# Optimization experiments

Hardware: AMD Instinct MI355X
Metric: run time of the kernel (lower is better)

Reference implementation:

```python
import jax, jax.numpy as jnp
import numpy as np
import math

MAX_L = 2
TARGET_DIM = 64


def build_transform_matrix(target_dim=TARGET_DIM, max_l=MAX_L):
    """Replicates WignerTransformMatrix._build_transform_matrix: [target_dim^2, 9]."""
    wigner_dims = [2 * l + 1 for l in range(max_l + 1)]  # [1, 3, 5]
    T = np.zeros((target_dim * target_dim, 9), dtype=np.float32)
    start = 0
    for l in range(max_l + 1):
        d = wigner_dims[l]
        if l == 0:
            for i in range(3):
                T[start, i * 3 + i] = 1.0 / 3.0
        elif l == 1:
            for i in range(d):
                for j in range(d):
                    T[start + i * d + j, i * 3 + j] = 1.0
        elif l == 2:
            for i in range(min(d, 3)):
                T[start + i * d + i, i * 3 + i] = 1.0
            rules = [(0, 1, [(0, 1, 0.5), (1, 0, 0.5)]),
                     (0, 2, [(0, 2, 0.7), (2, 0, 0.3)]),
                     (1, 2, [(1, 2, 0.6), (2, 1, 0.4)]),
                     (0, 4, [(0, 1, 0.3), (1, 0, 0.3), (0, 2, 0.2), (2, 0, 0.2)])]
            for oi, oj, combos in rules:
                if oi < d and oj < d:
                    for ii, jj, w in combos:
                        T[start + oi * d + oj, ii * 3 + jj] = w
                        if oi != oj:
                            T[start + oj * d + oi, ii * 3 + jj] = w
        start += d * d
    return jnp.asarray(T)


def setup_inputs() -> dict:
    key = jax.random.key(0)
    ks = jax.random.split(key, 12)
    B, N, H, G, D = 2, 1024, 8, 2, 64
    s = 0.02
    return {
        "x": jax.random.normal(ks[0], (B, N, H, G, D), dtype=jnp.float32),
        "rotations": jax.random.normal(ks[1], (B, N, 3, 3), dtype=jnp.float32),
        "mask": jnp.ones((B, N), dtype=bool),
        "Wq": jax.random.normal(ks[2], (D, D), dtype=jnp.float32) * s,
        "bq": jnp.zeros((D,), dtype=jnp.float32),
        "Wk": jax.random.normal(ks[3], (D, D), dtype=jnp.float32) * s,
        "bk": jnp.zeros((D,), dtype=jnp.float32),
        "Wv": jax.random.normal(ks[4], (D, D), dtype=jnp.float32) * s,
        "bv": jnp.zeros((D,), dtype=jnp.float32),
        "Wo": jax.random.normal(ks[5], (D, D), dtype=jnp.float32) * s,
        "bo": jnp.zeros((D,), dtype=jnp.float32),
        "fusion_weight": jnp.ones((1,), dtype=jnp.float32),
    }


def reference(x, rotations, mask, Wq, bq, Wk, bk, Wv, bv, Wo, bo, fusion_weight):
    B, N, H, G, D = x.shape
    HG = H * G
    scale = math.sqrt(D)
    T = build_transform_matrix(D, MAX_L)  # [D*D, 9]

    # projections (torch Linear: x @ W.T + b)
    q = (x @ Wq.T + bq).reshape(B, N, HG, D).transpose(0, 2, 1, 3)  # [B,HG,N,D]
    k = (x @ Wk.T + bk).reshape(B, N, HG, D).transpose(0, 2, 1, 3)
    v = (x @ Wv.T + bv).reshape(B, N, HG, D).transpose(0, 2, 1, 3)

    scores = jnp.einsum('bhnd,bhmd->bhnm', q, k) / scale  # [B,HG,N,N]

    # Wigner matrices: vec(R) @ T.T -> [B,N,D,D]
    R_vec = rotations.reshape(B, N, 9)
    wig = (R_vec @ T.T).reshape(B, N, D, D)

    # per-token transformed q/k (no [B,HG,N,D,D] materialization)
    q_t = jnp.einsum('bhnd,bnde->bhne', q, wig)
    k_t = jnp.einsum('bhnd,bnde->bhne', k, wig)
    wigner_scores = jnp.einsum('bhnd,bhmd->bhnm', q_t, k_t) / scale

    enhanced = scores + fusion_weight[0] * wigner_scores
    mask2d = mask[:, None, :, None] & mask[:, None, None, :]  # [B,1,N,N]
    enhanced = jnp.where(mask2d, enhanced, -jnp.inf)

    attn = jax.nn.softmax(enhanced, axis=-1)
    out = jnp.einsum('bhnm,bhmd->bhnd', attn, v)  # [B,HG,N,D]
    out = out.transpose(0, 2, 1, 3).reshape(B, N, H, G, D)
    return out @ Wo.T + bo
```

## Files before the change

### kernel.cpp

```cpp
#include <hip/hip_runtime.h>
#include <cstring>
#include <cstddef>

#define NB  2
#define NN  1024
#define NHG 16
#define ND  64

typedef unsigned short ushort_t;
typedef __attribute__((ext_vector_type(8))) short short8v;
typedef __attribute__((ext_vector_type(16))) float f32x16;

struct MMat { float m[81]; };

#define L2E 1.44269504088896f

__device__ inline unsigned cvt_pk_bf16(float a, float b) {
  unsigned r;
  asm("v_cvt_pk_bf16_f32 %0, %1, %2" : "=v"(r) : "v"(a), "v"(b));
  return r;
}
__device__ inline void split_pair(float a, float b, unsigned& hw, unsigned& lw) {
  hw = cvt_pk_bf16(a, b);
  float ah = __uint_as_float(hw << 16);
  float bh = __uint_as_float(hw & 0xffff0000u);
  lw = cvt_pk_bf16(a - ah, b - bh);
}

__device__ inline f32x16 mfma32(short8v a, short8v b, f32x16 c) {
  return __builtin_amdgcn_mfma_f32_32x32x16_bf16(a, b, c, 0, 0, 0);
}

__device__ inline void gl_lds16(const ushort_t* g, ushort_t* l) {
  __builtin_amdgcn_global_load_lds(
      (const __attribute__((address_space(1))) void*)g,
      (__attribute__((address_space(3))) void*)l, 16, 0, 0);
}

static void compute_M(float* M) {
  static float T[4096][9];
  std::memset(T, 0, sizeof(T));
  int start = 0;
  for (int l = 0; l <= 2; ++l) {
    int d = 2 * l + 1;
    if (l == 0) {
      for (int i = 0; i < 3; ++i) T[start][i * 3 + i] = 1.0f / 3.0f;
    } else if (l == 1) {
      for (int i = 0; i < d; ++i)
        for (int j = 0; j < d; ++j)
          T[start + i * d + j][i * 3 + j] = 1.0f;
    } else {
      for (int i = 0; i < 3; ++i) T[start + i * d + i][i * 3 + i] = 1.0f;
      const int   oiA[4] = {0, 0, 1, 0}, ojA[4] = {1, 2, 2, 4};
      const int   cnt_[4] = {2, 2, 2, 4};
      const int   iiA[4][4] = {{0,1,0,0},{0,2,0,0},{1,2,0,0},{0,1,0,2}};
      const int   jjA[4][4] = {{1,0,0,0},{2,0,0,0},{2,1,0,0},{1,0,2,0}};
      const float wA[4][4]  = {{0.5f,0.5f,0,0},{0.7f,0.3f,0,0},{0.6f,0.4f,0,0},{0.3f,0.3f,0.2f,0.2f}};
      for (int r = 0; r < 4; ++r) {
        int oi = oiA[r], oj = ojA[r];
        if (oi < d && oj < d) {
          for (int c = 0; c < cnt_[r]; ++c) {
            T[start + oi * d + oj][iiA[r][c] * 3 + jjA[r][c]] = wA[r][c];
            if (oi != oj) T[start + oj * d + oi][iiA[r][c] * 3 + jjA[r][c]] = wA[r][c];
          }
        }
      }
    }
    start += d * d;
  }
  for (int i = 0; i < 9; ++i)
    for (int j = 0; j < 9; ++j) {
      double a = 0.0;
      for (int f = 0; f < 4096; ++f) a += (double)T[f][i] * (double)T[f][j];
      M[i * 9 + j] = (float)a;
    }
}

__global__ __launch_bounds__(256) void qkv_gemm(
    const float* __restrict__ x, const float* __restrict__ rot,
    const float* __restrict__ fusion,
    const float* __restrict__ Wq, const float* __restrict__ bq,
    const float* __restrict__ Wk, const float* __restrict__ bk,
    const float* __restrict__ Wv, const float* __restrict__ bv,
    ushort_t* __restrict__ Qb, ushort_t* __restrict__ Kb,
    ushort_t* __restrict__ VhT, MMat Mm) {
  const int tid = threadIdx.x;
  const int w = tid >> 6, l = tid & 63;
  const int l31 = l & 31, hi5 = l >> 5;
  const int mt = blockIdx.x, p = blockIdx.y;
  const int bh = mt >> 3, n0 = (mt & 7) << 7;
  const float* W    = p == 0 ? Wq : (p == 1 ? Wk : Wv);
  const float* bvec = p == 0 ? bq : (p == 1 ? bk : bv);

  __shared__ union UU {
    struct { ushort_t A[128 * 72]; ushort_t B[2][64 * 72]; } s;
    float D[128 * 67];
  } u;
  __shared__ float biasS[64];
  __shared__ float rotS[128][9];

  #pragma unroll
  for (int it = 0; it < 8; ++it) {
    int i = tid + it * 256;
    int r = i >> 4, c4 = i & 15;
    const float* src = x + (((size_t)((bh >> 4) * 1024 + n0 + r) * 16 + (bh & 15)) << 6) + (c4 << 2);
    float4 v = *(const float4*)src;
    uint2 hw = { cvt_pk_bf16(v.x, v.y), cvt_pk_bf16(v.z, v.w) };
    *(uint2*)(&u.s.A[r * 72 + c4 * 4]) = hw;
  }
  #pragma unroll
  for (int it = 0; it < 4; ++it) {
    int i = tid + it * 256;
    int r = i >> 4, c4 = i & 15;
    float4 v = *(const float4*)(W + ((size_t)i << 2));
    unsigned h0, l0, h1, l1;
    split_pair(v.x, v.y, h0, l0);
    split_pair(v.z, v.w, h1, l1);
    uint2 hw = { h0, h1 }, lw = { l0, l1 };
    *(uint2*)(&u.s.B[0][r * 72 + c4 * 4]) = hw;
    *(uint2*)(&u.s.B[1][r * 72 + c4 * 4]) = lw;
  }
  if (tid < 64) biasS[tid] = bvec[tid];
  if (p < 2) {
    for (int i = tid; i < 1152; i += 256) {
      int r = i / 9, c = i - r * 9;
      rotS[r][c] = rot[((size_t)((bh >> 4) * 1024 + n0 + r)) * 9 + c];
    }
  }
  __syncthreads();

  f32x16 acc0, acc1;
  #pragma unroll
  for (int r = 0; r < 16; ++r) { acc0[r] = 0.f; acc1[r] = 0.f; }
  const int mbase = w << 5;
  __builtin_amdgcn_s_setprio(1);
  #pragma unroll
  for (int s = 0; s < 4; ++s) {
    const int ko = s * 16 + 8 * hi5;
    short8v aH  = *(const short8v*)(&u.s.A[(mbase + l31) * 72 + ko]);
    short8v b0H = *(const short8v*)(&u.s.B[0][l31 * 72 + ko]);
    short8v b0L = *(const short8v*)(&u.s.B[1][l31 * 72 + ko]);
    short8v b1H = *(const short8v*)(&u.s.B[0][(32 + l31) * 72 + ko]);
    short8v b1L = *(const short8v*)(&u.s.B[1][(32 + l31) * 72 + ko]);
    acc0 = mfma32(aH, b0H, acc0);
    acc0 = mfma32(aH, b0L, acc0);
    acc1 = mfma32(aH, b1H, acc1);
    acc1 = mfma32(aH, b1L, acc1);
  }
  __builtin_amdgcn_s_setprio(0);
  __syncthreads();
  #pragma unroll
  for (int r = 0; r < 16; ++r) {
    int m = mbase + (r & 3) + 8 * (r >> 2) + 4 * hi5;
    u.D[m * 67 + l31]      = acc0[r];
    u.D[m * 67 + 32 + l31] = acc1[r];
  }
  __syncthreads();

  if (p < 2) {
    const int mloc = tid >> 1, dh = (tid & 1) << 5;
    ushort_t* dst = p ? Kb : Qb;
    const float scale = p ? 1.0f : 0.125f * L2E;
    const size_t rowo = ((size_t)bh * 1024 + n0 + mloc) * 80;
    #pragma unroll
    for (int j = 0; j < 4; ++j) {
      union { unsigned wd[4]; short8v v; } pk;
      #pragma unroll
      for (int e = 0; e < 4; ++e) {
        int c = dh + 8 * j + 2 * e;
        float v0 = (u.D[mloc * 67 + c]     + biasS[c])     * scale;
        float v1 = (u.D[mloc * 67 + c + 1] + biasS[c + 1]) * scale;
        pk.wd[e] = cvt_pk_bf16(v0, v1);
      }
      *(short8v*)(dst + rowo + dh + 8 * j) = pk.v;
    }
    if (dh == 0) {
      float base0 = u.D[mloc * 67] + biasS[0];
      float e16[16];
      if (p == 0) {
        float fq = fusion[0] * base0 * (0.125f * L2E);
        #pragma unroll
        for (int j = 0; j < 16; ++j) e16[j] = (j < 9) ? fq * rotS[mloc][j] : 0.f;
      } else {
        #pragma unroll
        for (int j = 0; j < 16; ++j) {
          float a = 0.f;
          if (j < 9) {
            #pragma unroll
            for (int jj = 0; jj < 9; ++jj)
              a = fmaf(Mm.m[j * 9 + jj], rotS[mloc][jj], a);
          }
          e16[j] = base0 * a;
        }
      }
      union { unsigned wd[4]; short8v v; } pa, pb;
      #pragma unroll
      for (int e = 0; e < 4; ++e) {
        pa.wd[e] = cvt_pk_bf16(e16[2 * e], e16[2 * e + 1]);
        pb.wd[e] = cvt_pk_bf16(e16[8 + 2 * e], e16[9 + 2 * e]);
      }
      *(short8v*)(dst + rowo + 64) = pa.v;
      *(short8v*)(dst + rowo + 72) = pb.v;
    }
  } else {
    const int d = tid >> 2, nb = tid & 3;
    const float bd = biasS[d];
    const size_t ob = ((size_t)bh * 64 + d) * 1024 + n0;
    #pragma unroll
    for (int j = 0; j < 4; ++j) {
      int chunk = nb * 4 + j;
      union { unsigned wd[4]; short8v v; } pk;
      #pragma unroll
      for (int e = 0; e < 4; ++e) {
        int c = chunk * 8 + 2 * e;
        float v0 = u.D[c * 67 + d] + bd;
        float v1 = u.D[(c + 1) * 67 + d] + bd;
        pk.wd[e] = cvt_pk_bf16(v0, v1);
      }
      int slot = (chunk & 8) | ((chunk & 7) ^ (d & 7));
      *(short8v*)(VhT + ob + slot * 8) = pk.v;
    }
  }
}

__global__ __launch_bounds__(256, 4) void attn_kernel(
    const ushort_t* __restrict__ Qb, const ushort_t* __restrict__ Kb,
    const ushort_t* __restrict__ VhT,
    unsigned* __restrict__ OpartW, float* __restrict__ Ml, int SPLIT, int KTN) {
  const int tid = threadIdx.x;
  const int w = tid >> 6, l = tid & 63;
  const int l31 = l & 31, hi5 = l >> 5;
  const int bid = blockIdx.x;
  const int bh = bid & 31, rest = bid >> 5;
  const int qt = rest & 7, sp = rest >> 3;
  const int qn0 = qt * 128 + w * 32;
  const int sl = l31 & 7;

  __shared__ ushort_t Ks[2][64 * 80];
  __shared__ ushort_t Vs[2][64 * 64];

  short8v qh[5];
  {
    const ushort_t* qrow = Qb + ((size_t)bh * 1024 + qn0 + l31) * 80;
    #pragma unroll
    for (int s = 0; s < 5; ++s)
      qh[s] = *(const short8v*)(qrow + 16 * s + 8 * hi5);
  }

  f32x16 Ob0, Ob1;
  #pragma unroll
  for (int r = 0; r < 16; ++r) { Ob0[r] = 0.f; Ob1[r] = 0.f; }
  float lsum = 0.f;

  const ushort_t* Kbase = Kb + (size_t)bh * 1024 * 80;
  const ushort_t* VhB = VhT + (size_t)bh * 65536;
  const int kv0 = sp * KTN * 64;

  auto stage = [&](int b, int kt) {
    const int kb = kv0 + kt * 64;
    #pragma unroll
    for (int j = 0; j < 3; ++j) {
      int i = tid + j * 256;
      if (i < 640)
        gl_lds16(Kbase + (size_t)(kb + i / 10) * 80 + (i % 10) * 8, &Ks[b][i * 8]);
    }
    #pragma unroll
    for (int j = 0; j < 2; ++j) {
      int i = tid + j * 256;
      gl_lds16(VhB + (size_t)(i >> 3) * 1024 + kb + (i & 7) * 8, &Vs[b][i * 8]);
    }
  };

  stage(0, 0);
  for (int kt = 0; kt < KTN; ++kt) {
    const int cur = kt & 1;
    const bool haveNext = (kt + 1 < KTN);
    if (haveNext) stage(cur ^ 1, kt + 1);
    if (!haveNext)  { asm volatile("s_waitcnt vmcnt(0)" ::: "memory"); }
    else if (w < 2) { asm volatile("s_waitcnt vmcnt(5)" ::: "memory"); }
    else            { asm volatile("s_waitcnt vmcnt(4)" ::: "memory"); }
    __builtin_amdgcn_sched_barrier(0);
    __builtin_amdgcn_s_barrier();

    f32x16 S0, S1;
    #pragma unroll
    for (int r = 0; r < 16; ++r) { S0[r] = 0.f; S1[r] = 0.f; }
    __builtin_amdgcn_s_setprio(1);
    #pragma unroll
    for (int s = 0; s < 5; ++s) {
      short8v ka0 = *(const short8v*)(&Ks[cur][l31 * 80 + (2 * s + hi5) * 8]);
      S0 = mfma32(ka0, qh[s], S0);
      short8v ka1 = *(const short8v*)(&Ks[cur][(32 + l31) * 80 + (2 * s + hi5) * 8]);
      S1 = mfma32(ka1, qh[s], S1);
    }
    __builtin_amdgcn_s_setprio(0);

    float p0[16], p1[16];
    float ps = 0.f;
    #pragma unroll
    for (int r = 0; r < 16; ++r) {
      p0[r] = __builtin_amdgcn_exp2f(S0[r]);
      p1[r] = __builtin_amdgcn_exp2f(S1[r]);
      ps += p0[r] + p1[r];
    }
    lsum += ps;

    #pragma unroll
    for (int B = 0; B < 2; ++B) {
      const float* pp = (B == 0) ? p0 : p1;
      unsigned wh[8];
      #pragma unroll
      for (int i = 0; i < 8; ++i) wh[i] = cvt_pk_bf16(pp[2 * i], pp[2 * i + 1]);
      __builtin_amdgcn_s_setprio(1);
      #pragma unroll
      for (int s = 0; s < 2; ++s) {
        unsigned a0 = wh[4 * s], a1 = wh[4 * s + 1];
        unsigned b0 = wh[4 * s + 2], b1 = wh[4 * s + 3];
        asm volatile("v_permlane32_swap_b32 %0, %1" : "+v"(a0), "+v"(b0));
        asm volatile("v_permlane32_swap_b32 %0, %1" : "+v"(a1), "+v"(b1));
        union U8 { short8v v; unsigned u[4]; } aph;
        aph.u[0] = a0; aph.u[1] = a1; aph.u[2] = b0; aph.u[3] = b1;
        int slot = 4 * B + 2 * s + hi5;
        short8v vH0 = *(const short8v*)(&Vs[cur][l31 * 64 + (slot ^ sl) * 8]);
        Ob0 = mfma32(aph.v, vH0, Ob0);
        short8v vH1 = *(const short8v*)(&Vs[cur][(32 + l31) * 64 + (slot ^ sl) * 8]);
        Ob1 = mfma32(aph.v, vH1, Ob1);
      }
      __builtin_amdgcn_s_setprio(0);
    }
    __builtin_amdgcn_s_barrier();
  }

  lsum += __shfl_xor(lsum, 32, 64);
  #pragma unroll
  for (int r = 0; r < 16; ++r) {
    int cr = (r & 3) + 8 * (r >> 2) + 4 * hi5;
    size_t rowb = ((size_t)(bh * 1024 + qn0 + cr) * SPLIT + sp) * 32;
    OpartW[rowb + l31] = cvt_pk_bf16(Ob0[r], Ob1[r]);
  }
  if (l < 32)
    Ml[(size_t)(bh * 1024 + qn0 + l) * SPLIT + sp] = lsum;
}

__global__ __launch_bounds__(256) void oproj_gemm(
    const unsigned* __restrict__ OpartW, const float* __restrict__ Ml,
    float* __restrict__ out,
    const float* __restrict__ Wo, const float* __restrict__ bo, int SPLIT) {
  const int tid = threadIdx.x;
  const int w = tid >> 6, l = tid & 63;
  const int l31 = l & 31, hi5 = l >> 5;
  const int m0 = blockIdx.x << 6;
  const int rh = (w & 1) << 5;
  const int ch = (w >> 1) << 5;

  __shared__ union UU {
    struct { ushort_t A[64 * 72]; ushort_t B[2][64 * 72]; } s;
    float D[64 * 67];
  } u;
  __shared__ float biasS[64];
  __shared__ float cf[64];

  if (tid < 64) {
    int row = m0 + tid;
    int n = (row >> 4) & 1023, hgb = row & 15, bb = row >> 14;
    size_t prow = ((size_t)(bb * 16 + hgb)) * 1024 + n;
    float lt = 0.f;
    for (int s = 0; s < SPLIT; ++s) lt += Ml[prow * SPLIT + s];
    cf[tid] = 1.0f / lt;
  }
  if (tid >= 192) biasS[tid - 192] = bo[tid - 192];
  __syncthreads();

  #pragma unroll
  for (int it = 0; it < 2; ++it) {
    int i = tid + it * 256;
    int r = i >> 3, q4 = i & 7;
    int row = m0 + r;
    int n = (row >> 4) & 1023, hgb = row & 15, bb = row >> 14;
    size_t prow = ((size_t)(bb * 16 + hgb)) * 1024 + n;
    float f[8] = {0.f, 0.f, 0.f, 0.f, 0.f, 0.f, 0.f, 0.f};
    for (int s = 0; s < SPLIT; ++s) {
      uint4 wv = *(const uint4*)(OpartW + (prow * SPLIT + s) * 32 + q4 * 4);
      unsigned wa[4] = { wv.x, wv.y, wv.z, wv.w };
      #pragma unroll
      for (int j = 0; j < 4; ++j) {
        f[j]     += __uint_as_float(wa[j] << 16);
        f[4 + j] += __uint_as_float(wa[j] & 0xffff0000u);
      }
    }
    float li = cf[r];
    #pragma unroll
    for (int j = 0; j < 8; ++j) f[j] *= li;
    uint2 lo = { cvt_pk_bf16(f[0], f[1]), cvt_pk_bf16(f[2], f[3]) };
    uint2 hi = { cvt_pk_bf16(f[4], f[5]), cvt_pk_bf16(f[6], f[7]) };
    *(uint2*)(&u.s.A[r * 72 + q4 * 4])      = lo;
    *(uint2*)(&u.s.A[r * 72 + 32 + q4 * 4]) = hi;
  }
  #pragma unroll
  for (int it = 0; it < 4; ++it) {
    int i = tid + it * 256;
    int r = i >> 4, c4 = i & 15;
    float4 v = *(const float4*)(Wo + ((size_t)i << 2));
    unsigned h0, l0, h1, l1;
    split_pair(v.x, v.y, h0, l0);
    split_pair(v.z, v.w, h1, l1);
    uint2 hw = { h0, h1 }, lw = { l0, l1 };
    *(uint2*)(&u.s.B[0][r * 72 + c4 * 4]) = hw;
    *(uint2*)(&u.s.B[1][r * 72 + c4 * 4]) = lw;
  }
  __syncthreads();

  f32x16 acc;
  #pragma unroll
  for (int r = 0; r < 16; ++r) acc[r] = 0.f;
  __builtin_amdgcn_s_setprio(1);
  #pragma unroll
  for (int s = 0; s < 4; ++s) {
    const int ko = s * 16 + 8 * hi5;
    short8v aH = *(const short8v*)(&u.s.A[(rh + l31) * 72 + ko]);
    short8v bH = *(const short8v*)(&u.s.B[0][(ch + l31) * 72 + ko]);
    short8v bL = *(const short8v*)(&u.s.B[1][(ch + l31) * 72 + ko]);
    acc = mfma32(aH, bH, acc);
    acc = mfma32(aH, bL, acc);
  }
  __builtin_amdgcn_s_setprio(0);
  __syncthreads();
  #pragma unroll
  for (int r = 0; r < 16; ++r) {
    int m = rh + (r & 3) + 8 * (r >> 2) + 4 * hi5;
    u.D[m * 67 + ch + l31] = acc[r];
  }
  __syncthreads();

  const int mloc = tid >> 2, q = tid & 3;
  float* orow = out + ((size_t)(m0 + mloc) << 6) + q * 16;
  #pragma unroll
  for (int j = 0; j < 4; ++j) {
    int c = q * 16 + 4 * j;
    float4 v;
    v.x = u.D[mloc * 67 + c + 0] + biasS[c + 0];
    v.y = u.D[mloc * 67 + c + 1] + biasS[c + 1];
    v.z = u.D[mloc * 67 + c + 2] + biasS[c + 2];
    v.w = u.D[mloc * 67 + c + 3] + biasS[c + 3];
    *(float4*)(orow + 4 * j) = v;
  }
}

extern "C" void kernel_launch(void* const* d_in, const int* in_sizes, int n_in,
                              void* d_out, int out_size, void* d_ws, size_t ws_size,
                              hipStream_t stream) {
  const float* x   = (const float*)d_in[0];
  const float* rot = (const float*)d_in[1];
  const float* Wq  = (const float*)d_in[3];
  const float* bq  = (const float*)d_in[4];
  const float* Wk  = (const float*)d_in[5];
  const float* bk  = (const float*)d_in[6];
  const float* Wv  = (const float*)d_in[7];
  const float* bv  = (const float*)d_in[8];
  const float* Wo  = (const float*)d_in[9];
  const float* bo  = (const float*)d_in[10];
  const float* fus = (const float*)d_in[11];
  float* out = (float*)d_out;
  char* ws = (char*)d_ws;

  ushort_t* Qb  = (ushort_t*)ws;
  ushort_t* Kb  = (ushort_t*)(ws + 5242880);
  ushort_t* VhT = (ushort_t*)(ws + 10485760);
  const size_t obase = 14680064;

  int SPLIT = 1;
  if (ws_size >= obase + 4 * 4325376) SPLIT = 4;
  else if (ws_size >= obase + 2 * 4325376) SPLIT = 2;
  const int KTN = 16 / SPLIT;
  unsigned* OpartW = (unsigned*)(ws + obase);
  float*    Ml     = (float*)(ws + obase + (size_t)4194304 * SPLIT);

  MMat Mm;
  compute_M(Mm.m);

  qkv_gemm<<<dim3(256, 3), 256, 0, stream>>>(x, rot, fus, Wq, bq, Wk, bk, Wv, bv,
                                             Qb, Kb, VhT, Mm);
  attn_kernel<<<256 * SPLIT, 256, 0, stream>>>(Qb, Kb, VhT, OpartW, Ml, SPLIT, KTN);
  oproj_gemm<<<512, 256, 0, stream>>>(OpartW, Ml, out, Wo, bo, SPLIT);
}
```

Baseline: 46.52 us.

## Process two query tiles per attention block to reuse staged K/V tiles

Each attention block now handles two 128-row query tiles (A and B) against the same staged K/V tiles in LDS. This halves the block count and the global-to-LDS K/V traffic per query row, at the cost of doubled accumulator registers, with launch bounds dropped from four to two blocks per CU. Separately, the output-projection kernel issues all split-partial loads before the Wo conversion and the normalizer reduction, so those global loads overlap that work.

```diff
diff --git a/kernel.cpp b/kernel.cpp
--- a/kernel.cpp
+++ b/kernel.cpp
@@ -223,7 +223,7 @@
   }
 }
 
-__global__ __launch_bounds__(256, 4) void attn_kernel(
+__global__ __launch_bounds__(256, 2) void attn_kernel(
     const ushort_t* __restrict__ Qb, const ushort_t* __restrict__ Kb,
     const ushort_t* __restrict__ VhT,
     unsigned* __restrict__ OpartW, float* __restrict__ Ml, int SPLIT, int KTN) {
@@ -232,28 +232,32 @@
   const int l31 = l & 31, hi5 = l >> 5;
   const int bid = blockIdx.x;
   const int bh = bid & 31, rest = bid >> 5;
-  const int qt = rest & 7, sp = rest >> 3;
-  const int qn0 = qt * 128 + w * 32;
+  const int qtp = rest & 3, sp = rest >> 2;
+  const int qn0A = qtp * 256 + w * 32;
+  const int qn0B = qn0A + 128;
   const int sl = l31 & 7;
 
   __shared__ ushort_t Ks[2][64 * 80];
   __shared__ ushort_t Vs[2][64 * 64];
 
-  short8v qh[5];
+  short8v qhA[5], qhB[5];
   {
-    const ushort_t* qrow = Qb + ((size_t)bh * 1024 + qn0 + l31) * 80;
-    #pragma unroll
-    for (int s = 0; s < 5; ++s)
-      qh[s] = *(const short8v*)(qrow + 16 * s + 8 * hi5);
-  }
-
-  f32x16 Ob0, Ob1;
-  #pragma unroll
-  for (int r = 0; r < 16; ++r) { Ob0[r] = 0.f; Ob1[r] = 0.f; }
-  float lsum = 0.f;
+    const ushort_t* qrA = Qb + ((size_t)bh * 1024 + qn0A + l31) * 80;
+    const ushort_t* qrB = Qb + ((size_t)bh * 1024 + qn0B + l31) * 80;
+    #pragma unroll
+    for (int s = 0; s < 5; ++s) {
+      qhA[s] = *(const short8v*)(qrA + 16 * s + 8 * hi5);
+      qhB[s] = *(const short8v*)(qrB + 16 * s + 8 * hi5);
+    }
+  }
+
+  f32x16 OA0, OA1, OB0, OB1;
+  #pragma unroll
+  for (int r = 0; r < 16; ++r) { OA0[r] = 0.f; OA1[r] = 0.f; OB0[r] = 0.f; OB1[r] = 0.f; }
+  float lsA = 0.f, lsB = 0.f;
 
   const ushort_t* Kbase = Kb + (size_t)bh * 1024 * 80;
-  const ushort_t* VhB = VhT + (size_t)bh * 65536;
+  const ushort_t* VhB_ = VhT + (size_t)bh * 65536;
   const int kv0 = sp * KTN * 64;
 
   auto stage = [&](int b, int kt) {
@@ -267,7 +271,7 @@
     #pragma unroll
     for (int j = 0; j < 2; ++j) {
       int i = tid + j * 256;
-      gl_lds16(VhB + (size_t)(i >> 3) * 1024 + kb + (i & 7) * 8, &Vs[b][i * 8]);
+      gl_lds16(VhB_ + (size_t)(i >> 3) * 1024 + kb + (i & 7) * 8, &Vs[b][i * 8]);
     }
   };
 
@@ -282,64 +286,84 @@
     __builtin_amdgcn_sched_barrier(0);
     __builtin_amdgcn_s_barrier();
 
-    f32x16 S0, S1;
-    #pragma unroll
-    for (int r = 0; r < 16; ++r) { S0[r] = 0.f; S1[r] = 0.f; }
+    f32x16 SA0, SA1, SB0, SB1;
+    #pragma unroll
+    for (int r = 0; r < 16; ++r) { SA0[r] = 0.f; SA1[r] = 0.f; SB0[r] = 0.f; SB1[r] = 0.f; }
     __builtin_amdgcn_s_setprio(1);
     #pragma unroll
     for (int s = 0; s < 5; ++s) {
       short8v ka0 = *(const short8v*)(&Ks[cur][l31 * 80 + (2 * s + hi5) * 8]);
-      S0 = mfma32(ka0, qh[s], S0);
+      SA0 = mfma32(ka0, qhA[s], SA0);
+      SB0 = mfma32(ka0, qhB[s], SB0);
       short8v ka1 = *(const short8v*)(&Ks[cur][(32 + l31) * 80 + (2 * s + hi5) * 8]);
-      S1 = mfma32(ka1, qh[s], S1);
+      SA1 = mfma32(ka1, qhA[s], SA1);
+      SB1 = mfma32(ka1, qhB[s], SB1);
     }
     __builtin_amdgcn_s_setprio(0);
 
-    float p0[16], p1[16];
-    float ps = 0.f;
+    float pA0[16], pA1[16], pB0[16], pB1[16];
+    float psA = 0.f, psB = 0.f;
     #pragma unroll
     for (int r = 0; r < 16; ++r) {
-      p0[r] = __builtin_amdgcn_exp2f(S0[r]);
-      p1[r] = __builtin_amdgcn_exp2f(S1[r]);
-      ps += p0[r] + p1[r];
-    }
-    lsum += ps;
+      pA0[r] = __builtin_amdgcn_exp2f(SA0[r]);
+      pA1[r] = __builtin_amdgcn_exp2f(SA1[r]);
+      psA += pA0[r] + pA1[r];
+      pB0[r] = __builtin_amdgcn_exp2f(SB0[r]);
+      pB1[r] = __builtin_amdgcn_exp2f(SB1[r]);
+      psB += pB0[r] + pB1[r];
+    }
+    lsA += psA;
+    lsB += psB;
 
     #pragma unroll
     for (int B = 0; B < 2; ++B) {
-      const float* pp = (B == 0) ? p0 : p1;
-      unsigned wh[8];
+      const float* ppA = (B == 0) ? pA0 : pA1;
+      const float* ppB = (B == 0) ? pB0 : pB1;
+      unsigned whA[8], whB[8];
       #pragma unroll
-      for (int i = 0; i < 8; ++i) wh[i] = cvt_pk_bf16(pp[2 * i], pp[2 * i + 1]);
+      for (int i = 0; i < 8; ++i) {
+        whA[i] = cvt_pk_bf16(ppA[2 * i], ppA[2 * i + 1]);
+        whB[i] = cvt_pk_bf16(ppB[2 * i], ppB[2 * i + 1]);
+      }
       __builtin_amdgcn_s_setprio(1);
       #pragma unroll
       for (int s = 0; s < 2; ++s) {
-        unsigned a0 = wh[4 * s], a1 = wh[4 * s + 1];
-        unsigned b0 = wh[4 * s + 2], b1 = wh[4 * s + 3];
-        asm volatile("v_permlane32_swap_b32 %0, %1" : "+v"(a0), "+v"(b0));
-        asm volatile("v_permlane32_swap_b32 %0, %1" : "+v"(a1), "+v"(b1));
-        union U8 { short8v v; unsigned u[4]; } aph;
-        aph.u[0] = a0; aph.u[1] = a1; aph.u[2] = b0; aph.u[3] = b1;
+        unsigned aA0 = whA[4 * s], aA1 = whA[4 * s + 1];
+        unsigned bA0 = whA[4 * s + 2], bA1 = whA[4 * s + 3];
+        asm volatile("v_permlane32_swap_b32 %0, %1" : "+v"(aA0), "+v"(bA0));
+        asm volatile("v_permlane32_swap_b32 %0, %1" : "+v"(aA1), "+v"(bA1));
+        unsigned aB0 = whB[4 * s], aB1 = whB[4 * s + 1];
+        unsigned bB0 = whB[4 * s + 2], bB1 = whB[4 * s + 3];
+        asm volatile("v_permlane32_swap_b32 %0, %1" : "+v"(aB0), "+v"(bB0));
+        asm volatile("v_permlane32_swap_b32 %0, %1" : "+v"(aB1), "+v"(bB1));
+        union U8 { short8v v; unsigned u[4]; } apA, apB;
+        apA.u[0] = aA0; apA.u[1] = aA1; apA.u[2] = bA0; apA.u[3] = bA1;
+        apB.u[0] = aB0; apB.u[1] = aB1; apB.u[2] = bB0; apB.u[3] = bB1;
         int slot = 4 * B + 2 * s + hi5;
         short8v vH0 = *(const short8v*)(&Vs[cur][l31 * 64 + (slot ^ sl) * 8]);
-        Ob0 = mfma32(aph.v, vH0, Ob0);
+        OA0 = mfma32(apA.v, vH0, OA0);
+        OB0 = mfma32(apB.v, vH0, OB0);
         short8v vH1 = *(const short8v*)(&Vs[cur][(32 + l31) * 64 + (slot ^ sl) * 8]);
-        Ob1 = mfma32(aph.v, vH1, Ob1);
+        OA1 = mfma32(apA.v, vH1, OA1);
+        OB1 = mfma32(apB.v, vH1, OB1);
       }
       __builtin_amdgcn_s_setprio(0);
     }
     __builtin_amdgcn_s_barrier();
   }
 
-  lsum += __shfl_xor(lsum, 32, 64);
+  lsA += __shfl_xor(lsA, 32, 64);
+  lsB += __shfl_xor(lsB, 32, 64);
   #pragma unroll
   for (int r = 0; r < 16; ++r) {
     int cr = (r & 3) + 8 * (r >> 2) + 4 * hi5;
-    size_t rowb = ((size_t)(bh * 1024 + qn0 + cr) * SPLIT + sp) * 32;
-    OpartW[rowb + l31] = cvt_pk_bf16(Ob0[r], Ob1[r]);
-  }
-  if (l < 32)
-    Ml[(size_t)(bh * 1024 + qn0 + l) * SPLIT + sp] = lsum;
+    size_t rowbA = ((size_t)(bh * 1024 + qn0A + cr) * SPLIT + sp) * 32;
+    OpartW[rowbA + l31] = cvt_pk_bf16(OA0[r], OA1[r]);
+    size_t rowbB = ((size_t)(bh * 1024 + qn0B + cr) * SPLIT + sp) * 32;
+    OpartW[rowbB + l31] = cvt_pk_bf16(OB0[r], OB1[r]);
+  }
+  if (l < 32) Ml[(size_t)(bh * 1024 + qn0A + l) * SPLIT + sp] = lsA;
+  else        Ml[(size_t)(bh * 1024 + qn0B + (l - 32)) * SPLIT + sp] = lsB;
 }
 
 __global__ __launch_bounds__(256) void oproj_gemm(
@@ -360,41 +384,20 @@
   __shared__ float biasS[64];
   __shared__ float cf[64];
 
-  if (tid < 64) {
-    int row = m0 + tid;
-    int n = (row >> 4) & 1023, hgb = row & 15, bb = row >> 14;
-    size_t prow = ((size_t)(bb * 16 + hgb)) * 1024 + n;
-    float lt = 0.f;
-    for (int s = 0; s < SPLIT; ++s) lt += Ml[prow * SPLIT + s];
-    cf[tid] = 1.0f / lt;
-  }
-  if (tid >= 192) biasS[tid - 192] = bo[tid - 192];
-  __syncthreads();
-
+  uint4 wv[2][4];
+  int rr[2];
   #pragma unroll
   for (int it = 0; it < 2; ++it) {
     int i = tid + it * 256;
     int r = i >> 3, q4 = i & 7;
+    rr[it] = r;
     int row = m0 + r;
     int n = (row >> 4) & 1023, hgb = row & 15, bb = row >> 14;
     size_t prow = ((size_t)(bb * 16 + hgb)) * 1024 + n;
-    float f[8] = {0.f, 0.f, 0.f, 0.f, 0.f, 0.f, 0.f, 0.f};
-    for (int s = 0; s < SPLIT; ++s) {
-      uint4 wv = *(const uint4*)(OpartW + (prow * SPLIT + s) * 32 + q4 * 4);
-      unsigned wa[4] = { wv.x, wv.y, wv.z, wv.w };
-      #pragma unroll
-      for (int j = 0; j < 4; ++j) {
-        f[j]     += __uint_as_float(wa[j] << 16);
-        f[4 + j] += __uint_as_float(wa[j] & 0xffff0000u);
-      }
-    }
-    float li = cf[r];
-    #pragma unroll
-    for (int j = 0; j < 8; ++j) f[j] *= li;
-    uint2 lo = { cvt_pk_bf16(f[0], f[1]), cvt_pk_bf16(f[2], f[3]) };
-    uint2 hi = { cvt_pk_bf16(f[4], f[5]), cvt_pk_bf16(f[6], f[7]) };
-    *(uint2*)(&u.s.A[r * 72 + q4 * 4])      = lo;
-    *(uint2*)(&u.s.A[r * 72 + 32 + q4 * 4]) = hi;
+    #pragma unroll
+    for (int s = 0; s < 4; ++s)
+      if (s < SPLIT)
+        wv[it][s] = *(const uint4*)(OpartW + (prow * SPLIT + s) * 32 + q4 * 4);
   }
   #pragma unroll
   for (int it = 0; it < 4; ++it) {
@@ -407,6 +410,42 @@
     uint2 hw = { h0, h1 }, lw = { l0, l1 };
     *(uint2*)(&u.s.B[0][r * 72 + c4 * 4]) = hw;
     *(uint2*)(&u.s.B[1][r * 72 + c4 * 4]) = lw;
+  }
+  if (tid < 64) {
+    int row = m0 + tid;
+    int n = (row >> 4) & 1023, hgb = row & 15, bb = row >> 14;
+    size_t prow = ((size_t)(bb * 16 + hgb)) * 1024 + n;
+    float lt = 0.f;
+    for (int s = 0; s < SPLIT; ++s) lt += Ml[prow * SPLIT + s];
+    cf[tid] = 1.0f / lt;
+  }
+  if (tid >= 192) biasS[tid - 192] = bo[tid - 192];
+  __syncthreads();
+
+  #pragma unroll
+  for (int it = 0; it < 2; ++it) {
+    int i = tid + it * 256;
+    int q4 = i & 7;
+    int r = rr[it];
+    float f[8] = {0.f, 0.f, 0.f, 0.f, 0.f, 0.f, 0.f, 0.f};
+    #pragma unroll
+    for (int s = 0; s < 4; ++s) {
+      if (s < SPLIT) {
+        unsigned wa[4] = { wv[it][s].x, wv[it][s].y, wv[it][s].z, wv[it][s].w };
+        #pragma unroll
+        for (int j = 0; j < 4; ++j) {
+          f[j]     += __uint_as_float(wa[j] << 16);
+          f[4 + j] += __uint_as_float(wa[j] & 0xffff0000u);
+        }
+      }
+    }
+    float li = cf[r];
+    #pragma unroll
+    for (int j = 0; j < 8; ++j) f[j] *= li;
+    uint2 lo = { cvt_pk_bf16(f[0], f[1]), cvt_pk_bf16(f[2], f[3]) };
+    uint2 hi = { cvt_pk_bf16(f[4], f[5]), cvt_pk_bf16(f[6], f[7]) };
+    *(uint2*)(&u.s.A[r * 72 + q4 * 4])      = lo;
+    *(uint2*)(&u.s.A[r * 72 + 32 + q4 * 4]) = hi;
   }
   __syncthreads();
 
@@ -480,6 +519,6 @@
 
   qkv_gemm<<<dim3(256, 3), 256, 0, stream>>>(x, rot, fus, Wq, bq, Wk, bk, Wv, bv,
                                              Qb, Kb, VhT, Mm);
-  attn_kernel<<<256 * SPLIT, 256, 0, stream>>>(Qb, Kb, VhT, OpartW, Ml, SPLIT, KTN);
+  attn_kernel<<<128 * SPLIT, 256, 0, stream>>>(Qb, Kb, VhT, OpartW, Ml, SPLIT, KTN);
   oproj_gemm<<<512, 256, 0, stream>>>(OpartW, Ml, out, Wo, bo, SPLIT);
 }
```

Result: no change. 46.04 us (-1.0%).
